# Optimization experiments

Measured on AMD Instinct MI355X. Metric: run time of the kernel, lower is better.

Reference implementation:

```python
import jax, jax.numpy as jnp
import numpy as np

CHUNK = 8  # 2 ** spatial_dim


def _chunk_conv(x, W, b):
    # Conv1d with kernel_size == stride == K is a blocked matmul.
    # x: [B, T, C], W: [O, C, K] (torch Conv1d layout), b: [O]
    B, T, C = x.shape
    K = W.shape[2]
    xr = x.reshape(B, T // K, K, C)
    return jnp.einsum('btkc,ock->bto', xr, W) + b


def setup_inputs() -> dict:
    key = jax.random.key(0)
    ks = jax.random.split(key, 8)
    B, T1 = 8, 32768
    M = T1 // 2                      # number of mixed ('2') tokens in penultimate layer
    T2 = M * CHUNK                   # last layer: 8 children per mixed token
    num_vocab, embed_dim = 3, 256
    conv_depth = embed_dim // CHUNK  # 32
    # penultimate layer: alternating mixed(2)/full(1) tokens, same layout for all samples
    val1 = jnp.broadcast_to(jnp.where(jnp.arange(T1) % 2 == 0, 2, 1).astype(jnp.int32), (B, T1))
    # last layer: all non-padding tokens in [1, num_vocab]
    val2 = jax.random.randint(ks[0], (B, T2), 1, num_vocab + 1, dtype=jnp.int32)
    value = jnp.concatenate([val1, val2], axis=1)
    depth = jnp.concatenate([jnp.full((B, T1), 4, jnp.int32), jnp.full((B, T2), 5, jnp.int32)], axis=1)
    position = jax.random.randint(ks[1], (B, T1 + T2, 3), 1, 64, dtype=jnp.int32)  # unused by forward
    emb1 = 0.02 * jax.random.normal(ks[2], (num_vocab + 1, conv_depth), jnp.float32)
    emb2 = 0.02 * jax.random.normal(ks[3], (num_vocab + 1, conv_depth), jnp.float32)
    W1 = 0.05 * jax.random.normal(ks[4], (embed_dim, conv_depth, CHUNK), jnp.float32)
    b1 = jnp.zeros((embed_dim,), jnp.float32)
    W2 = 0.05 * jax.random.normal(ks[5], (conv_depth, conv_depth, CHUNK), jnp.float32)
    b2 = jnp.zeros((conv_depth,), jnp.float32)
    return {"value": value, "depth": depth, "position": position,
            "emb1": emb1, "emb2": emb2, "W1": W1, "b1": b1, "W2": W2, "b2": b2}


def reference(value, depth, position, emb1, emb2, W1, b1, W2, b2):
    # Layer lengths (uniform across batch in setup_inputs, so the torch per-sample
    # packing loop reduces to static slicing).
    max_d = jnp.max(depth)
    L1 = int(np.asarray(jnp.sum(depth[0] == max_d - 1)))
    L2 = int(np.asarray(jnp.sum(depth[0] == max_d)))
    val1 = value[:, :L1]
    val2 = value[:, L1:L1 + L2]
    # padding_idx=0 -> row 0 is zero
    e1 = emb1.at[0].set(0.0)
    e2 = emb2.at[0].set(0.0)
    x = e1[val1]                              # [B, L1, C]
    y = _chunk_conv(e2[val2], W2, b2)         # [B, L2//K, C]
    C = x.shape[-1]
    # Masked substitution: x[val1==2] = y[val2[:, ::K] != 0], matched in row-major rank order.
    m1 = (val1 == 2).reshape(-1)
    m2 = (val2[:, ::CHUNK] != 0).reshape(-1)
    yf = y.reshape(-1, C)
    rank2 = jnp.cumsum(m2) - 1
    # pack selected y rows densely by rank; out-of-bounds scatter indices are dropped
    buf = jnp.zeros_like(yf).at[jnp.where(m2, rank2, m2.size)].set(yf)
    rank1 = jnp.cumsum(m1) - 1
    sub = buf[jnp.clip(rank1, 0, m2.size - 1)]
    xf = jnp.where(m1[:, None], sub, x.reshape(-1, C))
    x = xf.reshape(x.shape[0], L1, C)
    return _chunk_conv(x, W1, b1)             # [B, L1//K, embed_dim]
```

## Files before the change

### kernel.cpp

```cpp
#include <hip/hip_runtime.h>
#include <hip/hip_bf16.h>


typedef short short8 __attribute__((ext_vector_type(8)));
typedef float f32x4 __attribute__((ext_vector_type(4)));

constexpr int TT_TOT = 163840;
constexpr int T1     = 32768;
constexpr int NU     = 4096;

__global__ __launch_bounds__(256) void prep_kernel(
    const float* __restrict__ emb1, const float* __restrict__ emb2,
    const float* __restrict__ W1,   const float* __restrict__ b1,
    const float* __restrict__ W2,   const float* __restrict__ b2,
    unsigned short* __restrict__ Tt)
{
    __shared__ float W2L[256 * 33];
    __shared__ float P[24 * 33];
    __shared__ float Wrow[256];
    __shared__ float E1[128], E2[128], B2[32];
    const int t = threadIdx.x;
    const int o = blockIdx.x;

    {
        #pragma unroll
        for (int c = 0; c < 32; ++c)
            W2L[t * 33 + c] = W2[c * 256 + t];
    }
    Wrow[t] = W1[o * 256 + t];
    if (t < 128) E1[t] = emb1[t];
    if (t >= 128 && t < 256) E2[t - 128] = emb2[t - 128];
    if (t < 32) B2[t] = b2[t];
    __syncthreads();

    #pragma unroll
    for (int i = 0; i < 3; ++i) {
        int idx = t + i * 256;
        int r = idx >> 5, c = idx & 31;
        int v1 = r >> 3, j = r & 7;
        float s = 0.f;
        #pragma unroll
        for (int cp = 0; cp < 32; ++cp)
            s += E2[(v1 + 1) * 32 + cp] * W2L[(cp * 8 + j) * 33 + c];
        P[r * 33 + c] = s;
    }
    __syncthreads();

    if (t < 128) {
        const int kap = t;
        float val = 0.f;
        if (kap < 96) {
            int v1 = kap >> 5, j = (kap >> 2) & 7, kk = kap & 3;
            #pragma unroll
            for (int c = 0; c < 32; ++c)
                val += P[(v1 * 8 + j) * 33 + c] * Wrow[c * 8 + 2 * kk];
        } else if (kap < 108) {
            int q = kap - 96; int v1 = q >> 2, ko = q & 3;
            #pragma unroll
            for (int c = 0; c < 32; ++c)
                val += E1[(v1 + 1) * 32 + c] * Wrow[c * 8 + 2 * ko + 1];
        } else if (kap == 108) {
            val = b1[o];
            #pragma unroll
            for (int kk = 0; kk < 4; ++kk)
                #pragma unroll
                for (int c = 0; c < 32; ++c)
                    val += B2[c] * Wrow[c * 8 + 2 * kk];
        }
        __hip_bfloat16 h = __float2bfloat16(val);
        Tt[o * 128 + kap] = *reinterpret_cast<unsigned short*>(&h);
    }
}

__global__ __launch_bounds__(256) void fused_kernel(
    const int* __restrict__ value,
    const unsigned short* __restrict__ Tt,
    float* __restrict__ out)
{
    __shared__ unsigned short Ind[64 * 128];
    const int t  = threadIdx.x;
    const int b  = blockIdx.x >> 6;
    const int u0 = (blockIdx.x & 63) * 64;
    const int lane = t & 63, w = t >> 6;
    const int m = lane & 15, quad = lane >> 4;
    const int row = t & 63, q = t >> 6;
    const int u = u0 + row;
    const int* vb = value + b * TT_TOT;

    const int* tok = vb + T1 + u * 32 + q * 8;
    const int4 ta  = *(const int4*)tok;
    const int4 tb2 = *(const int4*)(tok + 4);
    const int  v1tok = vb[u * 8 + 2 * q + 1];

    short8 tfrag[4][4];
    #pragma unroll
    for (int ot = 0; ot < 4; ++ot)
        #pragma unroll
        for (int ks = 0; ks < 4; ++ks)
            tfrag[ot][ks] = *(const short8*)(Tt + (w * 64 + ot * 16 + m) * 128
                                                + ks * 32 + quad * 8);

    #pragma unroll
    for (int i = 0; i < 4; ++i)
        ((uint4*)Ind)[t + i * 256] = make_uint4(0u, 0u, 0u, 0u);
    __syncthreads();

    {
        int vj[8] = {ta.x, ta.y, ta.z, ta.w, tb2.x, tb2.y, tb2.z, tb2.w};
        unsigned short* Ir = Ind + row * 128;
        const int rx = row & 7;
        #pragma unroll
        for (int j = 0; j < 8; ++j) {
            int v = vj[j];
            if (v > 0) {
                int slot = (v - 1) * 32 + j * 4 + q;
                Ir[(((slot >> 3) ^ rx) << 3) + (slot & 7)] = 0x3F80;
            }
        }
        if (v1tok > 0) {
            int slot = 96 + (v1tok - 1) * 4 + q;
            Ir[(((slot >> 3) ^ rx) << 3) + (slot & 7)] = 0x3F80;
        }
        if (q == 0) {
            int slot = 108;
            Ir[(((slot >> 3) ^ rx) << 3) + (slot & 7)] = 0x3F80;
        }
    }
    __syncthreads();

    f32x4 acc[4][4] = {};
    #pragma unroll
    for (int ut = 0; ut < 4; ++ut) {
        const int rl = ut * 16 + m;
        short8 ifrag[4];
        #pragma unroll
        for (int ks = 0; ks < 4; ++ks)
            ifrag[ks] = *(const short8*)&Ind[rl * 128 +
                              (((ks * 4 + quad) ^ (m & 7)) << 3)];
        #pragma unroll
        for (int ot = 0; ot < 4; ++ot)
            #pragma unroll
            for (int ks = 0; ks < 4; ++ks)
                acc[ot][ut] = __builtin_amdgcn_mfma_f32_16x16x32_bf16(
                    tfrag[ot][ks], ifrag[ks], acc[ot][ut], 0, 0, 0);
    }

    #pragma unroll
    for (int ut = 0; ut < 4; ++ut) {
        const int us = u0 + ut * 16 + m;
        #pragma unroll
        for (int ot = 0; ot < 4; ++ot) {
            float* op = out + ((b * NU + us) * 256) + w * 64 + ot * 16 + quad * 4;
            *(f32x4*)op = acc[ot][ut];
        }
    }
}

extern "C" void kernel_launch(void* const* d_in, const int* in_sizes, int n_in,
                              void* d_out, int out_size, void* d_ws, size_t ws_size,
                              hipStream_t stream)
{
    const int*   value = (const int*)  d_in[0];
    const float* emb1  = (const float*)d_in[3];
    const float* emb2  = (const float*)d_in[4];
    const float* W1    = (const float*)d_in[5];
    const float* b1    = (const float*)d_in[6];
    const float* W2    = (const float*)d_in[7];
    const float* b2    = (const float*)d_in[8];
    float* out = (float*)d_out;

    unsigned short* Tt = (unsigned short*)d_ws;

    prep_kernel<<<256, 256, 0, stream>>>(emb1, emb2, W1, b1, W2, b2, Tt);
    fused_kernel<<<512, 256, 0, stream>>>(value, Tt, out);
}
```

Before: 101.9 us.

## Merge prep and GEMM kernels into one launch with flag-based inter-block sync

```diff
diff --git a/kernel.cpp b/kernel.cpp
--- a/kernel.cpp
+++ b/kernel.cpp
@@ -8,79 +8,95 @@
 constexpr int TT_TOT = 163840;
 constexpr int T1     = 32768;
 constexpr int NU     = 4096;
-
-__global__ __launch_bounds__(256) void prep_kernel(
+constexpr unsigned MAGIC = 0x5A5A5A5Au;
+
+extern __shared__ char dynlds[];
+
+__global__ __launch_bounds__(256, 3) void mega_kernel(
+    const int*   __restrict__ value,
     const float* __restrict__ emb1, const float* __restrict__ emb2,
     const float* __restrict__ W1,   const float* __restrict__ b1,
     const float* __restrict__ W2,   const float* __restrict__ b2,
-    unsigned short* __restrict__ Tt)
+    unsigned short* __restrict__ Tt,
+    unsigned*       __restrict__ flags,
+    float*          __restrict__ out)
 {
-    __shared__ float W2L[256 * 33];
-    __shared__ float P[24 * 33];
-    __shared__ float Wrow[256];
-    __shared__ float E1[128], E2[128], B2[32];
     const int t = threadIdx.x;
-    const int o = blockIdx.x;
-
-    {
-        #pragma unroll
-        for (int c = 0; c < 32; ++c)
-            W2L[t * 33 + c] = W2[c * 256 + t];
-    }
-    Wrow[t] = W1[o * 256 + t];
-    if (t < 128) E1[t] = emb1[t];
-    if (t >= 128 && t < 256) E2[t - 128] = emb2[t - 128];
-    if (t < 32) B2[t] = b2[t];
-    __syncthreads();
-
-    #pragma unroll
-    for (int i = 0; i < 3; ++i) {
-        int idx = t + i * 256;
-        int r = idx >> 5, c = idx & 31;
-        int v1 = r >> 3, j = r & 7;
-        float s = 0.f;
-        #pragma unroll
-        for (int cp = 0; cp < 32; ++cp)
-            s += E2[(v1 + 1) * 32 + cp] * W2L[(cp * 8 + j) * 33 + c];
-        P[r * 33 + c] = s;
-    }
-    __syncthreads();
-
-    if (t < 128) {
-        const int kap = t;
-        float val = 0.f;
-        if (kap < 96) {
-            int v1 = kap >> 5, j = (kap >> 2) & 7, kk = kap & 3;
+
+    if (blockIdx.x < 256) {
+        float* W2L = (float*)dynlds;
+        __shared__ float P[24 * 33];
+        __shared__ float Wrow[256];
+        __shared__ float E1[128], E2[128], B2[32];
+        const int o = blockIdx.x;
+
+        Wrow[t] = W1[o * 256 + t];
+        if (t < 128) E1[t] = emb1[t];
+        if (t >= 128) E2[t - 128] = emb2[t - 128];
+        if (t < 32) B2[t] = b2[t];
+
+        for (int p = 0; p < 2; ++p) {
+            __syncthreads();
             #pragma unroll
-            for (int c = 0; c < 32; ++c)
-                val += P[(v1 * 8 + j) * 33 + c] * Wrow[c * 8 + 2 * kk];
-        } else if (kap < 108) {
-            int q = kap - 96; int v1 = q >> 2, ko = q & 3;
+            for (int i = 0; i < 16; ++i) {
+                int f = t + i * 256;
+                W2L[(f >> 8) * 257 + (f & 255)] = W2[p * 4096 + f];
+            }
+            __syncthreads();
             #pragma unroll
-            for (int c = 0; c < 32; ++c)
-                val += E1[(v1 + 1) * 32 + c] * Wrow[c * 8 + 2 * ko + 1];
-        } else if (kap == 108) {
-            val = b1[o];
-            #pragma unroll
-            for (int kk = 0; kk < 4; ++kk)
+            for (int i = 0; i < 2; ++i) {
+                int e = t + i * 256;
+                if (e < 384) {
+                    int r = e >> 4, cl = e & 15;
+                    int v1 = r >> 3, j = r & 7;
+                    float s = 0.f;
+                    #pragma unroll
+                    for (int cp = 0; cp < 32; ++cp)
+                        s += E2[(v1 + 1) * 32 + cp] * W2L[cl * 257 + cp * 8 + j];
+                    P[r * 33 + p * 16 + cl] = s;
+                }
+            }
+        }
+        __syncthreads();
+
+        if (t < 128) {
+            const int kap = t;
+            float val = 0.f;
+            if (kap < 96) {
+                int v1 = kap >> 5, j = (kap >> 2) & 7, kk = kap & 3;
                 #pragma unroll
                 for (int c = 0; c < 32; ++c)
-                    val += B2[c] * Wrow[c * 8 + 2 * kk];
-        }
-        __hip_bfloat16 h = __float2bfloat16(val);
-        Tt[o * 128 + kap] = *reinterpret_cast<unsigned short*>(&h);
-    }
-}
-
-__global__ __launch_bounds__(256) void fused_kernel(
-    const int* __restrict__ value,
-    const unsigned short* __restrict__ Tt,
-    float* __restrict__ out)
-{
-    __shared__ unsigned short Ind[64 * 128];
-    const int t  = threadIdx.x;
-    const int b  = blockIdx.x >> 6;
-    const int u0 = (blockIdx.x & 63) * 64;
+                    val += P[(v1 * 8 + j) * 33 + c] * Wrow[c * 8 + 2 * kk];
+            } else if (kap < 108) {
+                int q = kap - 96; int v1 = q >> 2, ko = q & 3;
+                #pragma unroll
+                for (int c = 0; c < 32; ++c)
+                    val += E1[(v1 + 1) * 32 + c] * Wrow[c * 8 + 2 * ko + 1];
+            } else if (kap == 108) {
+                val = b1[o];
+                #pragma unroll
+                for (int kk = 0; kk < 4; ++kk)
+                    #pragma unroll
+                    for (int c = 0; c < 32; ++c)
+                        val += B2[c] * Wrow[c * 8 + 2 * kk];
+            }
+            __hip_bfloat16 h = __float2bfloat16(val);
+            Tt[o * 128 + kap] = *reinterpret_cast<unsigned short*>(&h);
+        }
+
+        __syncthreads();
+        __threadfence();
+        __syncthreads();
+        if (t == 0)
+            __hip_atomic_store(&flags[o], MAGIC, __ATOMIC_RELEASE,
+                               __HIP_MEMORY_SCOPE_AGENT);
+        return;
+    }
+
+    unsigned short* Ind = (unsigned short*)dynlds;
+    const int gb = blockIdx.x - 256;
+    const int b  = gb >> 6;
+    const int u0 = (gb & 63) * 64;
     const int lane = t & 63, w = t >> 6;
     const int m = lane & 15, quad = lane >> 4;
     const int row = t & 63, q = t >> 6;
@@ -92,19 +108,10 @@
     const int4 tb2 = *(const int4*)(tok + 4);
     const int  v1tok = vb[u * 8 + 2 * q + 1];
 
-    short8 tfrag[4][4];
-    #pragma unroll
-    for (int ot = 0; ot < 4; ++ot)
-        #pragma unroll
-        for (int ks = 0; ks < 4; ++ks)
-            tfrag[ot][ks] = *(const short8*)(Tt + (w * 64 + ot * 16 + m) * 128
-                                                + ks * 32 + quad * 8);
-
     #pragma unroll
     for (int i = 0; i < 4; ++i)
         ((uint4*)Ind)[t + i * 256] = make_uint4(0u, 0u, 0u, 0u);
     __syncthreads();
-
     {
         int vj[8] = {ta.x, ta.y, ta.z, ta.w, tb2.x, tb2.y, tb2.z, tb2.w};
         unsigned short* Ir = Ind + row * 128;
@@ -127,6 +134,26 @@
         }
     }
     __syncthreads();
+
+    for (;;) {
+        unsigned good = 1u;
+        #pragma unroll
+        for (int i = 0; i < 4; ++i)
+            good &= (__hip_atomic_load(&flags[lane * 4 + i], __ATOMIC_RELAXED,
+                                       __HIP_MEMORY_SCOPE_AGENT) == MAGIC)
+                        ? 1u : 0u;
+        if (__ballot(good != 0u) == ~0ull) break;
+        __builtin_amdgcn_s_sleep(4);
+    }
+    __threadfence();
+
+    short8 tfrag[4][4];
+    #pragma unroll
+    for (int ot = 0; ot < 4; ++ot)
+        #pragma unroll
+        for (int ks = 0; ks < 4; ++ks)
+            tfrag[ot][ks] = *(const short8*)(Tt + (w * 64 + ot * 16 + m) * 128
+                                                + ks * 32 + quad * 8);
 
     f32x4 acc[4][4] = {};
     #pragma unroll
@@ -169,8 +196,9 @@
     const float* b2    = (const float*)d_in[8];
     float* out = (float*)d_out;
 
-    unsigned short* Tt = (unsigned short*)d_ws;
-
-    prep_kernel<<<256, 256, 0, stream>>>(emb1, emb2, W1, b1, W2, b2, Tt);
-    fused_kernel<<<512, 256, 0, stream>>>(value, Tt, out);
+    unsigned short* Tt    = (unsigned short*)d_ws;
+    unsigned*       flags = (unsigned*)((char*)d_ws + 65536);
+
+    mega_kernel<<<768, 256, 16448, stream>>>(
+        value, emb1, emb2, W1, b1, W2, b2, Tt, flags, out);
 }
```

Result: slower. 157.6 us (+54.6%).
